# Performance work log

Measured on AMD Instinct MI355X. Metric: run time of the kernel, lower is better.

The kernel has to match this reference:

```python
import jax, jax.numpy as jnp
import numpy as np

K = 3          # kernel_size
DIL = 2        # dilation
PAD = 2        # padding = dilation*(K-1)/2 so output spatial == input spatial
RANKS = 3
EPS = 1e-6


def _unfold(h):
    """Replicate-pad then extract KxK dilated patches -> (b, c, K*K, H, W).
    Kernel-position ordering matches torch.nn.Unfold (row-major kh*K+kw)."""
    b, c, H, W = h.shape
    p = jnp.pad(h, ((0, 0), (0, 0), (PAD, PAD), (PAD, PAD)), mode='edge')
    patches = [p[:, :, i * DIL:i * DIL + H, j * DIL:j * DIL + W]
               for i in range(K) for j in range(K)]
    return jnp.stack(patches, axis=2)  # (b, c, K*K, H, W)


def setup_inputs() -> dict:
    key = jax.random.key(0)
    k1, k2, k3 = jax.random.split(key, 3)
    B, C, H, W = 4, 64, 128, 128
    x = jax.random.normal(k1, (B, C, H, W), dtype=jnp.float32)
    W_head = jax.random.normal(k2, (64, 64), dtype=jnp.float32) * 0.05  # (out_c, in_c)
    W_tail = jax.random.normal(k3, (64, 64), dtype=jnp.float32) * 0.05  # (in_c, out_c)
    return {"x": x, "W_head": W_head, "W_tail": W_tail}


def reference(x, W_head, W_tail):
    res = x
    # 1x1 head conv (no bias) + ReLU
    h = jax.nn.relu(jnp.einsum('oc,bchw->bohw', W_head, x))
    # im2col: (b, C, K*K, H, W)
    X = _unfold(h)
    # NMF-style init: broadcast means over kernel / channel dims to rank r
    U = jnp.repeat(X.mean(axis=2, keepdims=True), RANKS, axis=2)  # (b,c,r,h,w)
    V = jnp.repeat(X.mean(axis=1, keepdims=True), RANKS, axis=1)  # (b,r,k,h,w)
    # one Lee-Seung multiplicative update (stage_num=1)
    num = jnp.einsum('bcrhw,bckhw->brkhw', U, X)
    den = jnp.einsum('bcrhw,bckhw->brkhw', U,
                     jnp.einsum('bcrhw,brkhw->bckhw', U, V))
    V = V * (num / (den + EPS))
    num = jnp.einsum('bckhw,brkhw->bcrhw', X, V)
    den = jnp.einsum('bckhw,brkhw->bcrhw',
                     jnp.einsum('bcrhw,brkhw->bckhw', U, V), V)
    U = U * (num / (den + EPS))
    center = (K // 2) * K + K // 2  # = 4
    UV = jnp.einsum('bcrhw,brkhw->bckhw', U, V[:, :, center:center + 1])[:, :, 0]
    out = jnp.einsum('co,bohw->bchw', W_tail, UV) + res
    return out
```

## Files before the change

kernel.cpp:

```cpp
#include <hip/hip_runtime.h>

#define HWC 16384
#define WD  128
#define NC  64
#define EPSV 1e-6f

typedef __attribute__((ext_vector_type(8))) short bf16x8;
typedef __attribute__((ext_vector_type(4))) float f32x4;

__device__ __forceinline__ unsigned short f2bf(float f) {
  unsigned u = __builtin_bit_cast(unsigned, f);
  u = (u + 0x7FFFu + ((u >> 16) & 1u)) >> 16;
  return (unsigned short)u;
}
__device__ __forceinline__ float bf2f(unsigned short h) {
  unsigned u = ((unsigned)h) << 16;
  return __builtin_bit_cast(float, u);
}
__device__ __forceinline__ float bfLo(unsigned pk) {
  return __builtin_bit_cast(float, pk << 16);
}
__device__ __forceinline__ float bfHi(unsigned pk) {
  return __builtin_bit_cast(float, pk & 0xFFFF0000u);
}
__device__ __forceinline__ int swz(int row, int colbytes) {
  return ((row << 7) + colbytes) ^ ((row & 7) << 4);
}

__global__ __launch_bounds__(256) void k_head(const float* __restrict__ x,
                                              const float* __restrict__ Wh,
                                              unsigned short* __restrict__ h) {
  __shared__ unsigned short whs[4096];
  __shared__ unsigned short xt[4096];
  const int t = threadIdx.x, lane = t & 63, wv = t >> 6;
  const int bid = blockIdx.x;
  const int seg = bid & 1, y = (bid >> 1) & 127, b = bid >> 8;
  const int w0 = seg << 6;

#pragma unroll
  for (int i = 0; i < 16; ++i) {
    const int idx = i * 256 + t;
    const int o = idx >> 6, c = idx & 63;
    *(unsigned short*)((char*)whs + swz(o, c * 2)) = f2bf(Wh[idx]);
  }
  {
    const float* xb = x + (size_t)b * (NC * HWC) + (size_t)y * WD + w0;
    const int c0 = wv << 4;
#pragma unroll
    for (int q = 0; q < 4; ++q) {
      unsigned long long pk = 0;
#pragma unroll
      for (int u = 0; u < 4; ++u) {
        const unsigned short v = f2bf(xb[(size_t)(c0 + q * 4 + u) * HWC + lane]);
        pk |= (unsigned long long)v << (16 * u);
      }
      *(unsigned long long*)((char*)xt + swz(lane, (c0 + q * 4) * 2)) = pk;
    }
  }
  __syncthreads();

  const int l15 = lane & 15, kg = lane >> 4;
  const int mrow = (wv << 4) + l15;
  const bf16x8 a0 = *(const bf16x8*)((char*)whs + swz(mrow, kg * 16));
  const bf16x8 a1 = *(const bf16x8*)((char*)whs + swz(mrow, 64 + kg * 16));
  const f32x4 z = {0.f, 0.f, 0.f, 0.f};
  unsigned short* hb = h + (size_t)b * (NC * HWC) + (size_t)y * WD + w0;
#pragma unroll
  for (int nt = 0; nt < 4; ++nt) {
    const int px = (nt << 4) + l15;
    const bf16x8 b0 = *(const bf16x8*)((char*)xt + swz(px, kg * 16));
    const bf16x8 b1 = *(const bf16x8*)((char*)xt + swz(px, 64 + kg * 16));
    f32x4 acc = __builtin_amdgcn_mfma_f32_16x16x32_bf16(a0, b0, z, 0, 0, 0);
    acc = __builtin_amdgcn_mfma_f32_16x16x32_bf16(a1, b1, acc, 0, 0, 0);
#pragma unroll
    for (int j = 0; j < 4; ++j) {
      const int o = (wv << 4) + kg * 4 + j;
      float v = acc[j];
      v = v > 0.f ? v : 0.f;
      hb[(size_t)o * HWC + px] = f2bf(v);
    }
  }
}

__global__ __launch_bounds__(512, 4) void k_nmf_tail(const unsigned short* __restrict__ h,
                                                     const float* __restrict__ x,
                                                     const float* __restrict__ Wt,
                                                     float* __restrict__ out) {
  __shared__ float red[512 * 21];
  __shared__ unsigned short wts[4096];
  unsigned short* uvb = (unsigned short*)red;

  const int t = threadIdx.x, lane = t & 63, wv = t >> 6;
  const int bid0 = blockIdx.x;
  const int bid = ((bid0 & 7) << 7) | (bid0 >> 3);
  const int seg = bid & 1, y = (bid >> 1) & 127, b = bid >> 8;
  const int w0 = seg << 6;

#pragma unroll
  for (int i = 0; i < 8; ++i) {
    const int idx = i * 512 + t;
    const int c = idx >> 6, o = idx & 63;
    *(unsigned short*)((char*)wts + swz(c, o * 2)) = f2bf(Wt[idx]);
  }

  const int wcol = w0 + lane;
  int aw = wcol - 2; if (aw < 0) aw = 0;
  int bw = wcol + 2; if (bw > 127) bw = 127;
  int rowoff[3];
  rowoff[0] = (y >= 2 ? y - 2 : 0) * WD;
  rowoff[1] = y * WD;
  rowoff[2] = (y <= 125 ? y + 2 : 127) * WD;

  const unsigned short* hb = h + (size_t)b * (NC * HWC);
  const int c0 = wv << 3;

  float S = 0.f, sumk[9], A[9], mreg[8];
  unsigned tp[8][5];
#pragma unroll
  for (int k = 0; k < 9; ++k) { sumk[k] = 0.f; A[k] = 0.f; }

#pragma unroll
  for (int i = 0; i < 8; ++i) {
    const unsigned short* hc = hb + (size_t)(c0 + i) * HWC;
    unsigned short t9[9];
#pragma unroll
    for (int r = 0; r < 3; ++r) {
      t9[3 * r + 0] = hc[rowoff[r] + aw];
      t9[3 * r + 1] = hc[rowoff[r] + wcol];
      t9[3 * r + 2] = hc[rowoff[r] + bw];
    }
    tp[i][0] = (unsigned)t9[0] | ((unsigned)t9[1] << 16);
    tp[i][1] = (unsigned)t9[2] | ((unsigned)t9[3] << 16);
    tp[i][2] = (unsigned)t9[4] | ((unsigned)t9[5] << 16);
    tp[i][3] = (unsigned)t9[6] | ((unsigned)t9[7] << 16);
    tp[i][4] = (unsigned)t9[8];
    float tap[9];
#pragma unroll
    for (int k = 0; k < 9; ++k) tap[k] = bf2f(t9[k]);
    float m = 0.f;
#pragma unroll
    for (int k = 0; k < 9; ++k) m += tap[k];
    m *= (1.f / 9.f);
    mreg[i] = m;
    S += m * m;
#pragma unroll
    for (int k = 0; k < 9; ++k) { sumk[k] += tap[k]; A[k] += m * tap[k]; }
  }

  {
    const int rb = t * 21;
    red[rb + 0] = S;
#pragma unroll
    for (int k = 0; k < 9; ++k) red[rb + 1 + k] = sumk[k];
#pragma unroll
    for (int k = 0; k < 9; ++k) red[rb + 10 + k] = A[k];
  }
  __syncthreads();

  for (int q = wv; q < 19; q += 8) {
    float f = 0.f;
#pragma unroll
    for (int w = 0; w < 8; ++w) f += red[(w * 64 + lane) * 21 + q];
    red[lane * 21 + q] = f;
  }
  __syncthreads();

  float Vk[9], T = 0.f;
  {
    const int rb = lane * 21;
    const float Sf = red[rb + 0];
#pragma unroll
    for (int k = 0; k < 9; ++k) {
      const float sk = red[rb + 1 + k];
      const float Ak = red[rb + 10 + k];
      const float nk = sk * (1.f / 64.f);
      Vk[k] = nk * (Ak / (3.f * nk * Sf + EPSV));
      T += Vk[k] * Vk[k];
    }
  }
  const float V4 = Vk[4];
  __syncthreads();

#pragma unroll
  for (int i = 0; i < 8; i += 2) {
    unsigned short pk[2];
#pragma unroll
    for (int u = 0; u < 2; ++u) {
      float Bc = 0.f;
      Bc += bfLo(tp[i + u][0]) * Vk[0];
      Bc += bfHi(tp[i + u][0]) * Vk[1];
      Bc += bfLo(tp[i + u][1]) * Vk[2];
      Bc += bfHi(tp[i + u][1]) * Vk[3];
      Bc += bfLo(tp[i + u][2]) * Vk[4];
      Bc += bfHi(tp[i + u][2]) * Vk[5];
      Bc += bfLo(tp[i + u][3]) * Vk[6];
      Bc += bfHi(tp[i + u][3]) * Vk[7];
      Bc += bfLo(tp[i + u][4]) * Vk[8];
      const float m = mreg[i + u];
      const float Uc = m * (Bc / (3.f * m * T + EPSV));
      pk[u] = f2bf(3.f * Uc * V4);
    }
    const unsigned w32 = (unsigned)pk[0] | ((unsigned)pk[1] << 16);
    *(unsigned*)((char*)uvb + swz(lane, (c0 + i) * 2)) = w32;
  }
  __syncthreads();

  const int l15 = lane & 15, kg = lane >> 4;
  const int mtile = wv & 3, n0 = (wv >> 2) << 1;
  const int mrow = (mtile << 4) + l15;
  const bf16x8 a0 = *(const bf16x8*)((char*)wts + swz(mrow, kg * 16));
  const bf16x8 a1 = *(const bf16x8*)((char*)wts + swz(mrow, 64 + kg * 16));
  const f32x4 z = {0.f, 0.f, 0.f, 0.f};
  const size_t gb = (size_t)b * (NC * HWC) + (size_t)y * WD + w0;
#pragma unroll
  for (int nt = n0; nt < n0 + 2; ++nt) {
    const int px = (nt << 4) + l15;
    const bf16x8 b0 = *(const bf16x8*)((char*)uvb + swz(px, kg * 16));
    const bf16x8 b1 = *(const bf16x8*)((char*)uvb + swz(px, 64 + kg * 16));
    f32x4 acc = __builtin_amdgcn_mfma_f32_16x16x32_bf16(a0, b0, z, 0, 0, 0);
    acc = __builtin_amdgcn_mfma_f32_16x16x32_bf16(a1, b1, acc, 0, 0, 0);
#pragma unroll
    for (int j = 0; j < 4; ++j) {
      const int c2 = (mtile << 4) + kg * 4 + j;
      const size_t off = gb + (size_t)c2 * HWC + px;
      out[off] = acc[j] + x[off];
    }
  }
}

extern "C" void kernel_launch(void* const* d_in, const int* in_sizes, int n_in,
                              void* d_out, int out_size, void* d_ws, size_t ws_size,
                              hipStream_t stream) {
  const float* x  = (const float*)d_in[0];
  const float* Wh = (const float*)d_in[1];
  const float* Wt = (const float*)d_in[2];
  float* out = (float*)d_out;
  unsigned short* h = (unsigned short*)d_ws;

  k_head<<<1024, 256, 0, stream>>>(x, Wh, h);
  k_nmf_tail<<<1024, 512, 0, stream>>>(h, x, Wt, out);
}
```

Baseline: 29.22 us.

## Fuse head conv into NMF tail kernel with halo recompute in shared memory

Merges the head 1x1 conv+ReLU kernel into the NMF/tail kernel. Each block now loads the three dilated input rows plus halo columns of x, computes h for them with MFMA into LDS, and reads taps from LDS. This removes the bf16 h round trip through global memory and one kernel launch. The cost is recomputing the head conv for neighbouring rows (about 3.3x head FLOPs and x reads). Weight fragments are also loaded straight from global into registers instead of staged through LDS.

```diff
diff --git a/kernel.cpp b/kernel.cpp
--- a/kernel.cpp
+++ b/kernel.cpp
@@ -14,120 +14,121 @@
   return (unsigned short)u;
 }
 __device__ __forceinline__ float bf2f(unsigned short h) {
-  unsigned u = ((unsigned)h) << 16;
-  return __builtin_bit_cast(float, u);
-}
-__device__ __forceinline__ float bfLo(unsigned pk) {
-  return __builtin_bit_cast(float, pk << 16);
-}
-__device__ __forceinline__ float bfHi(unsigned pk) {
-  return __builtin_bit_cast(float, pk & 0xFFFF0000u);
-}
+  return __builtin_bit_cast(float, ((unsigned)h) << 16);
+}
+__device__ __forceinline__ float bfLo(unsigned pk) { return __builtin_bit_cast(float, pk << 16); }
+__device__ __forceinline__ float bfHi(unsigned pk) { return __builtin_bit_cast(float, pk & 0xFFFF0000u); }
 __device__ __forceinline__ int swz(int row, int colbytes) {
   return ((row << 7) + colbytes) ^ ((row & 7) << 4);
 }
-
-__global__ __launch_bounds__(256) void k_head(const float* __restrict__ x,
-                                              const float* __restrict__ Wh,
-                                              unsigned short* __restrict__ h) {
-  __shared__ unsigned short whs[4096];
-  __shared__ unsigned short xt[4096];
-  const int t = threadIdx.x, lane = t & 63, wv = t >> 6;
-  const int bid = blockIdx.x;
-  const int seg = bid & 1, y = (bid >> 1) & 127, b = bid >> 8;
-  const int w0 = seg << 6;
-
-#pragma unroll
-  for (int i = 0; i < 16; ++i) {
-    const int idx = i * 256 + t;
-    const int o = idx >> 6, c = idx & 63;
-    *(unsigned short*)((char*)whs + swz(o, c * 2)) = f2bf(Wh[idx]);
-  }
-  {
-    const float* xb = x + (size_t)b * (NC * HWC) + (size_t)y * WD + w0;
-    const int c0 = wv << 4;
-#pragma unroll
-    for (int q = 0; q < 4; ++q) {
-      unsigned long long pk = 0;
-#pragma unroll
-      for (int u = 0; u < 4; ++u) {
-        const unsigned short v = f2bf(xb[(size_t)(c0 + q * 4 + u) * HWC + lane]);
-        pk |= (unsigned long long)v << (16 * u);
-      }
-      *(unsigned long long*)((char*)xt + swz(lane, (c0 + q * 4) * 2)) = pk;
-    }
-  }
-  __syncthreads();
-
-  const int l15 = lane & 15, kg = lane >> 4;
-  const int mrow = (wv << 4) + l15;
-  const bf16x8 a0 = *(const bf16x8*)((char*)whs + swz(mrow, kg * 16));
-  const bf16x8 a1 = *(const bf16x8*)((char*)whs + swz(mrow, 64 + kg * 16));
-  const f32x4 z = {0.f, 0.f, 0.f, 0.f};
-  unsigned short* hb = h + (size_t)b * (NC * HWC) + (size_t)y * WD + w0;
-#pragma unroll
-  for (int nt = 0; nt < 4; ++nt) {
-    const int px = (nt << 4) + l15;
-    const bf16x8 b0 = *(const bf16x8*)((char*)xt + swz(px, kg * 16));
-    const bf16x8 b1 = *(const bf16x8*)((char*)xt + swz(px, 64 + kg * 16));
-    f32x4 acc = __builtin_amdgcn_mfma_f32_16x16x32_bf16(a0, b0, z, 0, 0, 0);
-    acc = __builtin_amdgcn_mfma_f32_16x16x32_bf16(a1, b1, acc, 0, 0, 0);
-#pragma unroll
-    for (int j = 0; j < 4; ++j) {
-      const int o = (wv << 4) + kg * 4 + j;
-      float v = acc[j];
-      v = v > 0.f ? v : 0.f;
-      hb[(size_t)o * HWC + px] = f2bf(v);
-    }
-  }
-}
-
-__global__ __launch_bounds__(512, 4) void k_nmf_tail(const unsigned short* __restrict__ h,
-                                                     const float* __restrict__ x,
-                                                     const float* __restrict__ Wt,
-                                                     float* __restrict__ out) {
-  __shared__ float red[512 * 21];
-  __shared__ unsigned short wts[4096];
-  unsigned short* uvb = (unsigned short*)red;
+__device__ __forceinline__ bf16x8 pack8(float4 a, float4 b) {
+  bf16x8 r;
+  r[0] = (short)f2bf(a.x); r[1] = (short)f2bf(a.y);
+  r[2] = (short)f2bf(a.z); r[3] = (short)f2bf(a.w);
+  r[4] = (short)f2bf(b.x); r[5] = (short)f2bf(b.y);
+  r[6] = (short)f2bf(b.z); r[7] = (short)f2bf(b.w);
+  return r;
+}
+
+__global__ __launch_bounds__(512, 4) void k_fused(const float* __restrict__ x,
+                                                  const float* __restrict__ Wh,
+                                                  const float* __restrict__ Wt,
+                                                  float* __restrict__ out) {
+  __shared__ __align__(16) char smem[53760];
+  unsigned short* xt = (unsigned short*)smem;
+  unsigned short* hl = (unsigned short*)(smem + 26624);
+  float* red = (float*)smem;
+  unsigned short* uvb = (unsigned short*)smem;
 
   const int t = threadIdx.x, lane = t & 63, wv = t >> 6;
   const int bid0 = blockIdx.x;
   const int bid = ((bid0 & 7) << 7) | (bid0 >> 3);
   const int seg = bid & 1, y = (bid >> 1) & 127, b = bid >> 8;
   const int w0 = seg << 6;
-
-#pragma unroll
-  for (int i = 0; i < 8; ++i) {
-    const int idx = i * 512 + t;
-    const int c = idx >> 6, o = idx & 63;
-    *(unsigned short*)((char*)wts + swz(c, o * 2)) = f2bf(Wt[idx]);
-  }
-
-  const int wcol = w0 + lane;
-  int aw = wcol - 2; if (aw < 0) aw = 0;
-  int bw = wcol + 2; if (bw > 127) bw = 127;
-  int rowoff[3];
-  rowoff[0] = (y >= 2 ? y - 2 : 0) * WD;
-  rowoff[1] = y * WD;
-  rowoff[2] = (y <= 125 ? y + 2 : 127) * WD;
-
-  const unsigned short* hb = h + (size_t)b * (NC * HWC);
   const int c0 = wv << 3;
+  const int l15 = lane & 15, kg = lane >> 4;
+  const int mt = wv & 3;
+  const int mrow = (mt << 4) + l15;
+
+  int gy[3];
+  gy[0] = y >= 2 ? y - 2 : 0;
+  gy[1] = y;
+  gy[2] = y <= 125 ? y + 2 : 127;
+
+  const float* xb = x + (size_t)b * (NC * HWC);
+
+  bf16x8 ha0, ha1;
+  {
+    const float* wr = Wh + mrow * 64 + kg * 8;
+    ha0 = pack8(*(const float4*)wr, *(const float4*)(wr + 4));
+    ha1 = pack8(*(const float4*)(wr + 32), *(const float4*)(wr + 36));
+  }
+
+  {
+    int colm = w0 - 2 + lane; if (colm < 0) colm = 0;
+#pragma unroll
+    for (int r = 0; r < 3; ++r) {
+      const float* xr = xb + gy[r] * WD;
+      const int srow = r * 68 + lane;
+#pragma unroll
+      for (int q = 0; q < 2; ++q) {
+        unsigned long long pk = 0;
+#pragma unroll
+        for (int u = 0; u < 4; ++u)
+          pk |= (unsigned long long)f2bf(xr[(size_t)(c0 + q * 4 + u) * HWC + colm]) << (16 * u);
+        *(unsigned long long*)((char*)xt + swz(srow, (c0 + q * 4) * 2)) = pk;
+      }
+    }
+    if (lane < 12) {
+      const int re = lane >> 2, e = lane & 3;
+      int cole = w0 + 62 + e; if (cole > 127) cole = 127;
+      const float* xr = xb + gy[re] * WD;
+      const int srow = re * 68 + 64 + e;
+#pragma unroll
+      for (int q = 0; q < 2; ++q) {
+        unsigned long long pk = 0;
+#pragma unroll
+        for (int u = 0; u < 4; ++u)
+          pk |= (unsigned long long)f2bf(xr[(size_t)(c0 + q * 4 + u) * HWC + cole]) << (16 * u);
+        *(unsigned long long*)((char*)xt + swz(srow, (c0 + q * 4) * 2)) = pk;
+      }
+    }
+  }
+  __syncthreads();
+
+  {
+    const int ntBeg = (wv >> 2) ? 7 : 0;
+    const int ntEnd = (wv >> 2) ? 13 : 7;
+    const f32x4 z = {0.f, 0.f, 0.f, 0.f};
+    for (int nt = ntBeg; nt < ntEnd; ++nt) {
+      const int s = (nt << 4) + l15;
+      const bf16x8 b0 = *(const bf16x8*)((char*)xt + swz(s, kg * 16));
+      const bf16x8 b1 = *(const bf16x8*)((char*)xt + swz(s, 64 + kg * 16));
+      f32x4 acc = __builtin_amdgcn_mfma_f32_16x16x32_bf16(ha0, b0, z, 0, 0, 0);
+      acc = __builtin_amdgcn_mfma_f32_16x16x32_bf16(ha1, b1, acc, 0, 0, 0);
+#pragma unroll
+      for (int j = 0; j < 4; ++j) {
+        const int c2 = (mt << 4) + kg * 4 + j;
+        float v = acc[j];
+        v = v > 0.f ? v : 0.f;
+        hl[c2 * 212 + s] = f2bf(v);
+      }
+    }
+  }
+  __syncthreads();
 
   float S = 0.f, sumk[9], A[9], mreg[8];
   unsigned tp[8][5];
 #pragma unroll
   for (int k = 0; k < 9; ++k) { sumk[k] = 0.f; A[k] = 0.f; }
-
 #pragma unroll
   for (int i = 0; i < 8; ++i) {
-    const unsigned short* hc = hb + (size_t)(c0 + i) * HWC;
+    const int hb2 = (c0 + i) * 212 + lane;
     unsigned short t9[9];
 #pragma unroll
     for (int r = 0; r < 3; ++r) {
-      t9[3 * r + 0] = hc[rowoff[r] + aw];
-      t9[3 * r + 1] = hc[rowoff[r] + wcol];
-      t9[3 * r + 2] = hc[rowoff[r] + bw];
+#pragma unroll
+      for (int k = 0; k < 3; ++k) t9[3 * r + k] = hl[hb2 + r * 68 + 2 * k];
     }
     tp[i][0] = (unsigned)t9[0] | ((unsigned)t9[1] << 16);
     tp[i][1] = (unsigned)t9[2] | ((unsigned)t9[3] << 16);
@@ -146,6 +147,7 @@
 #pragma unroll
     for (int k = 0; k < 9; ++k) { sumk[k] += tap[k]; A[k] += m * tap[k]; }
   }
+  __syncthreads();
 
   {
     const int rb = t * 21;
@@ -180,6 +182,13 @@
   }
   const float V4 = Vk[4];
   __syncthreads();
+
+  bf16x8 ta0, ta1;
+  {
+    const float* wr = Wt + mrow * 64 + kg * 8;
+    ta0 = pack8(*(const float4*)wr, *(const float4*)(wr + 4));
+    ta1 = pack8(*(const float4*)(wr + 32), *(const float4*)(wr + 36));
+  }
 
 #pragma unroll
   for (int i = 0; i < 8; i += 2) {
@@ -205,11 +214,7 @@
   }
   __syncthreads();
 
-  const int l15 = lane & 15, kg = lane >> 4;
-  const int mtile = wv & 3, n0 = (wv >> 2) << 1;
-  const int mrow = (mtile << 4) + l15;
-  const bf16x8 a0 = *(const bf16x8*)((char*)wts + swz(mrow, kg * 16));
-  const bf16x8 a1 = *(const bf16x8*)((char*)wts + swz(mrow, 64 + kg * 16));
+  const int n0 = (wv >> 2) << 1;
   const f32x4 z = {0.f, 0.f, 0.f, 0.f};
   const size_t gb = (size_t)b * (NC * HWC) + (size_t)y * WD + w0;
 #pragma unroll
@@ -217,11 +222,11 @@
     const int px = (nt << 4) + l15;
     const bf16x8 b0 = *(const bf16x8*)((char*)uvb + swz(px, kg * 16));
     const bf16x8 b1 = *(const bf16x8*)((char*)uvb + swz(px, 64 + kg * 16));
-    f32x4 acc = __builtin_amdgcn_mfma_f32_16x16x32_bf16(a0, b0, z, 0, 0, 0);
-    acc = __builtin_amdgcn_mfma_f32_16x16x32_bf16(a1, b1, acc, 0, 0, 0);
+    f32x4 acc = __builtin_amdgcn_mfma_f32_16x16x32_bf16(ta0, b0, z, 0, 0, 0);
+    acc = __builtin_amdgcn_mfma_f32_16x16x32_bf16(ta1, b1, acc, 0, 0, 0);
 #pragma unroll
     for (int j = 0; j < 4; ++j) {
-      const int c2 = (mtile << 4) + kg * 4 + j;
+      const int c2 = (mt << 4) + kg * 4 + j;
       const size_t off = gb + (size_t)c2 * HWC + px;
       out[off] = acc[j] + x[off];
     }
@@ -235,8 +240,6 @@
   const float* Wh = (const float*)d_in[1];
   const float* Wt = (const float*)d_in[2];
   float* out = (float*)d_out;
-  unsigned short* h = (unsigned short*)d_ws;
-
-  k_head<<<1024, 256, 0, stream>>>(x, Wh, h);
-  k_nmf_tail<<<1024, 512, 0, stream>>>(h, x, Wt, out);
-}
+
+  k_fused<<<1024, 512, 0, stream>>>(x, Wh, Wt, out);
+}
```

New measurement: 28.10 us. 3.8% less time.
